# Kernel optimization log

Hardware: AMD Instinct MI355X
Metric: run time of the kernel (lower is better)

## Reference

```python
import jax, jax.numpy as jnp
import numpy as np

N_NODES = 50000
N_EDGES = 800000
N_FEAT = 128
HIDDEN = 128
N_CLASSES = 10
N_LAYERS = 3
N_GRAPHS = 512


def setup_inputs() -> dict:
    key = jax.random.key(0)
    ks = jax.random.split(key, 16)
    s = 1.0 / np.sqrt(HIDDEN)
    inp = {
        "x": jax.random.normal(ks[0], (N_NODES, N_FEAT), jnp.float32),
        "edge_index": jax.random.randint(ks[1], (2, N_EDGES), 0, N_NODES, jnp.int64),
        "batch": jnp.sort(jax.random.randint(ks[2], (N_NODES,), 0, N_GRAPHS, jnp.int64)),
        "num_graphs": N_GRAPHS,
        "conv1_wl": jax.random.normal(ks[3], (N_FEAT, HIDDEN), jnp.float32) * s,
        "conv1_wr": jax.random.normal(ks[4], (N_FEAT, HIDDEN), jnp.float32) * s,
        "conv1_b": jnp.zeros((HIDDEN,), jnp.float32),
        "convs_wl": jax.random.normal(ks[5], (N_LAYERS - 1, HIDDEN, HIDDEN), jnp.float32) * s,
        "convs_wr": jax.random.normal(ks[6], (N_LAYERS - 1, HIDDEN, HIDDEN), jnp.float32) * s,
        "convs_b": jnp.zeros((N_LAYERS - 1, HIDDEN), jnp.float32),
        "gate_w": jax.random.normal(ks[7], (HIDDEN, 1), jnp.float32) * s,
        "gate_b": jnp.zeros((1,), jnp.float32),
        "lin1_w": jax.random.normal(ks[8], (HIDDEN, HIDDEN), jnp.float32) * s,
        "lin1_b": jnp.zeros((HIDDEN,), jnp.float32),
        "lin2_w": jax.random.normal(ks[9], (HIDDEN, N_CLASSES), jnp.float32) * s,
        "lin2_b": jnp.zeros((N_CLASSES,), jnp.float32),
    }
    return inp


def _sage_conv(x, src, dst, inv_deg, wl, wr, b):
    # mean aggregation of source-node features at destination nodes
    agg = jax.ops.segment_sum(x[src], dst, num_segments=N_NODES)  # [N, d]
    agg = agg * inv_deg
    return agg @ wl + x @ wr + b


def _global_attention(x, batch, num_graphs, gate_w, gate_b):
    gate = (x @ gate_w + gate_b)[:, 0]                      # [N]
    m = jax.ops.segment_max(gate, batch, num_segments=num_graphs)
    m = jnp.where(jnp.isfinite(m), m, 0.0)
    g = jnp.exp(gate - m[batch])                            # stable segment softmax
    den = jax.ops.segment_sum(g, batch, num_segments=num_graphs)
    attn = g / den[batch]
    return jax.ops.segment_sum(attn[:, None] * x, batch, num_segments=num_graphs)


def reference(x, edge_index, batch, num_graphs,
              conv1_wl, conv1_wr, conv1_b,
              convs_wl, convs_wr, convs_b,
              gate_w, gate_b, lin1_w, lin1_b, lin2_w, lin2_b):
    src, dst = edge_index[0], edge_index[1]
    deg = jax.ops.segment_sum(jnp.ones((src.shape[0],), x.dtype), dst,
                              num_segments=N_NODES)
    inv_deg = (1.0 / jnp.maximum(deg, 1.0))[:, None]

    h = jax.nn.relu(_sage_conv(x, src, dst, inv_deg, conv1_wl, conv1_wr, conv1_b))
    for i in range(convs_wl.shape[0]):
        h = jax.nn.relu(_sage_conv(h, src, dst, inv_deg,
                                   convs_wl[i], convs_wr[i], convs_b[i]))

    pooled = _global_attention(h, batch, num_graphs, gate_w, gate_b)  # [G, H]
    out = jax.nn.relu(pooled @ lin1_w + lin1_b)
    # dropout p=0.5 is identity at eval time
    logits = out @ lin2_w + lin2_b
    return jax.nn.log_softmax(logits, axis=-1)
```

## Files before the change

### kernel.cpp

```cpp
#include <hip/hip_runtime.h>
#include <math.h>

#define N_NODES 50000
#define N_PAD   50048
#define N_EDGES 800000
#define FEAT 128
#define K2 256
#define N_GRAPHS 512
#define N_CLASSES 10
#define BCAP 64
#define RANGE_SZ 12500

typedef __attribute__((ext_vector_type(8))) short short8;
typedef __attribute__((ext_vector_type(4))) float floatx4;

__device__ __forceinline__ float bflo(unsigned u) { return __uint_as_float(u << 16); }
__device__ __forceinline__ float bfhi(unsigned u) { return __uint_as_float(u & 0xffff0000u); }
__device__ __forceinline__ unsigned short f2bf(float f) {
    unsigned u = __float_as_uint(f);
    u = (u + 0x7fffu + ((u >> 16) & 1u)) >> 16;
    return (unsigned short)u;
}
__device__ __forceinline__ unsigned pack2(float a, float b) {
    return (unsigned)f2bf(a) | ((unsigned)f2bf(b) << 16);
}
__device__ __forceinline__ unsigned fkey(float f) {
    unsigned b = __float_as_uint(f);
    return (b & 0x80000000u) ? ~b : (b | 0x80000000u);
}
__device__ __forceinline__ float fdecode(unsigned k) {
    unsigned b = (k & 0x80000000u) ? (k ^ 0x80000000u) : ~k;
    return __uint_as_float(b);
}

__global__ __launch_bounds__(256) void fill_bucket(
    const int* __restrict__ src, const int* __restrict__ dst,
    int* __restrict__ cnt, unsigned short* __restrict__ bucket) {
    int range = blockIdx.x & 3;
    int chunk = blockIdx.x >> 2;
    int e = chunk * 256 + threadIdx.x;
    int lo = range * RANGE_SZ;
    int d = dst[e];
    if (d >= lo && d < lo + RANGE_SZ) {
        int p = atomicAdd(&cnt[d], 1);
        if (p < BCAP) bucket[(size_t)d * BCAP + p] = (unsigned short)src[e];
    }
}

__global__ __launch_bounds__(256) void setup_kernel(
    const float* __restrict__ x, unsigned short* __restrict__ A,
    const float* __restrict__ wl1, const float* __restrict__ wr1,
    const float* __restrict__ wl23, const float* __restrict__ wr23,
    unsigned short* __restrict__ wt,
    const int* __restrict__ batch, int* __restrict__ goffs) {
    int b = blockIdx.x;
    if (b < 6250) {
        int idx = b * 256 + threadIdx.x;
        if (idx < N_NODES * 32) {
            int n = idx >> 5, f4 = idx & 31;
            float4 v = ((const float4*)(x + (size_t)n * FEAT))[f4];
            uint2 o = make_uint2(pack2(v.x, v.y), pack2(v.z, v.w));
            *(uint2*)(A + (size_t)n * K2 + FEAT + f4 * 4) = o;
        }
    } else if (b < 6250 + 384) {
        int idx = (b - 6250) * 256 + threadIdx.x;
        int layer = idx >> 15;
        int r = idx & 32767;
        int n = r >> 8, k = r & 255;
        const float* wl = (layer == 0) ? wl1 : wl23 + (size_t)(layer - 1) * FEAT * FEAT;
        const float* wr = (layer == 0) ? wr1 : wr23 + (size_t)(layer - 1) * FEAT * FEAT;
        float v = (k < FEAT) ? wl[k * FEAT + n] : wr[(k - FEAT) * FEAT + n];
        wt[idx] = f2bf(v);
    } else {
        int g = (b - 6250 - 384) * 256 + threadIdx.x;
        if (g > N_GRAPHS) return;
        int lo = 0, hi = N_NODES;
        while (lo < hi) {
            int mid = (lo + hi) >> 1;
            if (batch[mid] < g) lo = mid + 1; else hi = mid;
        }
        goffs[g] = lo;
    }
}

__device__ __forceinline__ void acc8(float* acc, uint4 u) {
    acc[0] += bflo(u.x); acc[1] += bfhi(u.x);
    acc[2] += bflo(u.y); acc[3] += bfhi(u.y);
    acc[4] += bflo(u.z); acc[5] += bfhi(u.z);
    acc[6] += bflo(u.w); acc[7] += bfhi(u.w);
}

__global__ __launch_bounds__(256) void aggregate_bf16(
    const unsigned short* __restrict__ hin, const int* __restrict__ cnt,
    const unsigned short* __restrict__ bucket, unsigned short* __restrict__ aggout) {
    int n = blockIdx.x * 4 + (threadIdx.x >> 6);
    if (n >= N_NODES) return;
    int lane = threadIdx.x & 63;
    int g = lane >> 4;
    int l16 = lane & 15;
    int deg = cnt[n];
    int c = min(deg, BCAP);
    int nq = c >> 2;
    int rem = c & 3;
    const unsigned short* cp = bucket + (size_t)n * BCAP;

    float acc[8];
    #pragma unroll
    for (int i = 0; i < 8; ++i) acc[i] = 0.f;

    int i = 0;
    for (; i + 4 <= nq; i += 4) {
        int s0 = cp[i * 4 + g];
        int s1 = cp[i * 4 + 4 + g];
        int s2 = cp[i * 4 + 8 + g];
        int s3 = cp[i * 4 + 12 + g];
        uint4 u0 = *(const uint4*)(hin + (size_t)s0 * K2 + l16 * 8);
        uint4 u1 = *(const uint4*)(hin + (size_t)s1 * K2 + l16 * 8);
        uint4 u2 = *(const uint4*)(hin + (size_t)s2 * K2 + l16 * 8);
        uint4 u3 = *(const uint4*)(hin + (size_t)s3 * K2 + l16 * 8);
        acc8(acc, u0); acc8(acc, u1); acc8(acc, u2); acc8(acc, u3);
    }
    if (i + 2 <= nq) {
        int s0 = cp[i * 4 + g];
        int s1 = cp[i * 4 + 4 + g];
        uint4 u0 = *(const uint4*)(hin + (size_t)s0 * K2 + l16 * 8);
        uint4 u1 = *(const uint4*)(hin + (size_t)s1 * K2 + l16 * 8);
        acc8(acc, u0); acc8(acc, u1);
        i += 2;
    }
    if (i < nq) {
        int s0 = cp[i * 4 + g];
        uint4 u0 = *(const uint4*)(hin + (size_t)s0 * K2 + l16 * 8);
        acc8(acc, u0);
    }
    if (g < rem) {
        int s0 = cp[nq * 4 + g];
        uint4 u0 = *(const uint4*)(hin + (size_t)s0 * K2 + l16 * 8);
        acc8(acc, u0);
    }
    #pragma unroll
    for (int j = 0; j < 8; ++j) {
        acc[j] += __shfl_xor(acc[j], 16);
        acc[j] += __shfl_xor(acc[j], 32);
    }
    if (g == 0) {
        float inv = 1.0f / fmaxf((float)deg, 1.0f);
        uint4 o;
        o.x = pack2(acc[0] * inv, acc[1] * inv);
        o.y = pack2(acc[2] * inv, acc[3] * inv);
        o.z = pack2(acc[4] * inv, acc[5] * inv);
        o.w = pack2(acc[6] * inv, acc[7] * inv);
        *(uint4*)(aggout + (size_t)n * K2 + l16 * 8) = o;
    }
}

__global__ __launch_bounds__(256) void gemm_mfma(
    unsigned short* __restrict__ A, const unsigned short* __restrict__ Wt,
    const float* __restrict__ bias,
    const float* __restrict__ gate_w, float* __restrict__ gate,
    unsigned* __restrict__ gmax, const int* __restrict__ batch) {
    int wave = threadIdx.x >> 6, lane = threadIdx.x & 63;
    int q = lane >> 4, l16 = lane & 15;
    int row0 = blockIdx.x * 128 + wave * 32;
    const unsigned short* pa0 = A + (size_t)(row0 + l16) * K2 + q * 8;
    const unsigned short* pa1 = pa0 + 16 * K2;
    const unsigned short* pb  = Wt + (size_t)l16 * K2 + q * 8;

    floatx4 acc[2][8];
    #pragma unroll
    for (int i = 0; i < 2; ++i)
        #pragma unroll
        for (int j = 0; j < 8; ++j) acc[i][j] = (floatx4){0.f, 0.f, 0.f, 0.f};

    #pragma unroll
    for (int ks = 0; ks < 8; ++ks) {
        short8 a0 = *(const short8*)(pa0 + ks * 32);
        short8 a1 = *(const short8*)(pa1 + ks * 32);
        #pragma unroll
        for (int nb = 0; nb < 8; ++nb) {
            short8 b = *(const short8*)(pb + (size_t)nb * 16 * K2 + ks * 32);
            acc[0][nb] = __builtin_amdgcn_mfma_f32_16x16x32_bf16(a0, b, acc[0][nb], 0, 0, 0);
            acc[1][nb] = __builtin_amdgcn_mfma_f32_16x16x32_bf16(a1, b, acc[1][nb], 0, 0, 0);
        }
    }

    float bv[8], gwv[8];
    #pragma unroll
    for (int nb = 0; nb < 8; ++nb) bv[nb] = bias[nb * 16 + l16];
    if (gate_w) {
        #pragma unroll
        for (int nb = 0; nb < 8; ++nb) gwv[nb] = gate_w[nb * 16 + l16];
    }

    #pragma unroll
    for (int band = 0; band < 2; ++band) {
        #pragma unroll
        for (int r = 0; r < 4; ++r) {
            int m = row0 + band * 16 + q * 4 + r;
            float gsum = 0.f;
            #pragma unroll
            for (int nb = 0; nb < 8; ++nb) {
                float v = fmaxf(acc[band][nb][r] + bv[nb], 0.f);
                if (m < N_NODES) A[(size_t)m * K2 + FEAT + nb * 16 + l16] = f2bf(v);
                if (gate_w) gsum += v * gwv[nb];
            }
            if (gate_w) {
                gsum += __shfl_xor(gsum, 1);
                gsum += __shfl_xor(gsum, 2);
                gsum += __shfl_xor(gsum, 4);
                gsum += __shfl_xor(gsum, 8);
                if (l16 == 0 && m < N_NODES) {
                    gate[m] = gsum;
                    atomicMax(&gmax[batch[m]], fkey(gsum));
                }
            }
        }
    }
}

__global__ __launch_bounds__(256) void pool_head(
    const unsigned short* __restrict__ h, const float* __restrict__ gate,
    const unsigned* __restrict__ gmax, const int* __restrict__ goffs,
    const float* __restrict__ w1, const float* __restrict__ b1,
    const float* __restrict__ w2, const float* __restrict__ b2,
    float* __restrict__ out) {
    __shared__ float sred[4];
    __shared__ float facc[4][128];
    __shared__ float pv[128], qv[128], lg[N_CLASSES];
    int g = blockIdx.x;
    int s = goffs[g], e = goffs[g + 1];
    int t = threadIdx.x;
    int wave = t >> 6, lane = t & 63;

    if (s < e) {
        float m = fdecode(gmax[g]);
        float d = 0.f;
        for (int n = s + t; n < e; n += 256) d += __expf(gate[n] - m);
        #pragma unroll
        for (int off = 32; off; off >>= 1) d += __shfl_xor(d, off);
        if (lane == 0) sred[wave] = d;
        __syncthreads();
        float den = sred[0] + sred[1] + sred[2] + sred[3];
        float acc0 = 0.f, acc1 = 0.f;
        for (int n = s + wave; n < e; n += 4) {
            float gn = __expf(gate[n] - m);
            unsigned u = *(const unsigned*)(h + (size_t)n * K2 + lane * 2);
            acc0 += gn * bflo(u);
            acc1 += gn * bfhi(u);
        }
        facc[wave][lane * 2]     = acc0;
        facc[wave][lane * 2 + 1] = acc1;
        __syncthreads();
        if (t < 128) pv[t] = (facc[0][t] + facc[1][t] + facc[2][t] + facc[3][t]) / den;
    } else {
        if (t < 128) pv[t] = 0.f;
    }
    __syncthreads();

    if (t < 128) {
        float acc = b1[t];
        #pragma unroll 4
        for (int k = 0; k < 128; ++k) acc += pv[k] * w1[k * FEAT + t];
        qv[t] = fmaxf(acc, 0.f);
    }
    __syncthreads();
    if (t < N_CLASSES) {
        float a = b2[t];
        #pragma unroll 4
        for (int k = 0; k < 128; ++k) a += qv[k] * w2[k * N_CLASSES + t];
        lg[t] = a;
    }
    __syncthreads();
    if (t < N_CLASSES) {
        float m = -INFINITY;
        #pragma unroll
        for (int j = 0; j < N_CLASSES; ++j) m = fmaxf(m, lg[j]);
        float sum = 0.f;
        #pragma unroll
        for (int j = 0; j < N_CLASSES; ++j) sum += __expf(lg[j] - m);
        out[(size_t)g * N_CLASSES + t] = lg[t] - m - __logf(sum);
    }
}

static inline size_t align256(size_t x) { return (x + 255) & ~(size_t)255; }

extern "C" void kernel_launch(void* const* d_in, const int* in_sizes, int n_in,
                              void* d_out, int out_size, void* d_ws, size_t ws_size,
                              hipStream_t stream) {
    const float* x        = (const float*)d_in[0];
    const int*   ei       = (const int*)d_in[1];
    const int*   batch    = (const int*)d_in[2];
    const float* conv1_wl = (const float*)d_in[4];
    const float* conv1_wr = (const float*)d_in[5];
    const float* conv1_b  = (const float*)d_in[6];
    const float* convs_wl = (const float*)d_in[7];
    const float* convs_wr = (const float*)d_in[8];
    const float* convs_b  = (const float*)d_in[9];
    const float* gate_w   = (const float*)d_in[10];
    const float* lin1_w   = (const float*)d_in[12];
    const float* lin1_b   = (const float*)d_in[13];
    const float* lin2_w   = (const float*)d_in[14];
    const float* lin2_b   = (const float*)d_in[15];
    float* out = (float*)d_out;

    const int* src = ei;
    const int* dst = ei + N_EDGES;

    char* w = (char*)d_ws;
    size_t off = 0;
    unsigned short* A1   = (unsigned short*)(w + off); off += align256((size_t)N_PAD * K2 * 2);
    unsigned short* bkt  = (unsigned short*)(w + off); off += align256((size_t)N_NODES * BCAP * 2);
    unsigned short* wt   = (unsigned short*)(w + off); off += align256((size_t)3 * FEAT * K2 * 2);
    float* f_gate = (float*)(w + off); off += align256((size_t)N_NODES * 4);
    int*   i_goff = (int*)(w + off);   off += align256((size_t)(N_GRAPHS + 1) * 4);
    char* zbase = w + off;
    int*      i_cnt  = (int*)(w + off);      off += align256((size_t)N_NODES * 4);
    unsigned* u_gmax = (unsigned*)(w + off); off += align256((size_t)N_GRAPHS * 4);
    size_t zbytes = (size_t)((w + off) - zbase);

    hipMemsetAsync(zbase, 0, zbytes, stream);

    fill_bucket<<<12500, 256, 0, stream>>>(src, dst, i_cnt, bkt);
    setup_kernel<<<6250 + 384 + 3, 256, 0, stream>>>(
        x, A1, conv1_wl, conv1_wr, convs_wl, convs_wr, wt, batch, i_goff);

    const int AB = (N_NODES + 3) / 4;
    const int GB = N_PAD / 128;

    aggregate_bf16<<<AB, 256, 0, stream>>>(A1 + FEAT, i_cnt, bkt, A1);
    gemm_mfma<<<GB, 256, 0, stream>>>(A1, wt, conv1_b,
                                      nullptr, nullptr, nullptr, nullptr);
    aggregate_bf16<<<AB, 256, 0, stream>>>(A1 + FEAT, i_cnt, bkt, A1);
    gemm_mfma<<<GB, 256, 0, stream>>>(A1, wt + FEAT * K2, convs_b,
                                      nullptr, nullptr, nullptr, nullptr);
    aggregate_bf16<<<AB, 256, 0, stream>>>(A1 + FEAT, i_cnt, bkt, A1);
    gemm_mfma<<<GB, 256, 0, stream>>>(A1, wt + 2 * FEAT * K2, convs_b + FEAT,
                                      gate_w, f_gate, u_gmax, batch);

    pool_head<<<N_GRAPHS, 256, 0, stream>>>(A1 + FEAT, f_gate, u_gmax, i_goff,
                                            lin1_w, lin1_b, lin2_w, lin2_b, out);
}
```

Before: 352.3 us.

## Make GEMM persistent with weights staged in LDS and prefetched A tiles

The GEMM kernel becomes persistent: 256 blocks loop over 64-row tiles. Each block copies the 128x256 bf16 weight matrix into padded shared memory once, instead of reading B fragments from global memory for every tile. The A fragments for the next tile are prefetched into registers while the current tile's MFMAs run. This cuts repeated weight traffic and launch granularity. In exchange it uses about 66KB of LDS per block, which limits occupancy, and it processes fewer rows per wave.

```diff
diff --git a/kernel.cpp b/kernel.cpp
--- a/kernel.cpp
+++ b/kernel.cpp
@@ -10,6 +10,10 @@
 #define N_CLASSES 10
 #define BCAP 64
 #define RANGE_SZ 12500
+#define WROW 264
+#define TILE_ROWS 64
+#define GEMM_BLOCKS 256
+#define N_TILES 782
 
 typedef __attribute__((ext_vector_type(8))) short short8;
 typedef __attribute__((ext_vector_type(4))) float floatx4;
@@ -159,29 +163,17 @@
     const float* __restrict__ bias,
     const float* __restrict__ gate_w, float* __restrict__ gate,
     unsigned* __restrict__ gmax, const int* __restrict__ batch) {
-    int wave = threadIdx.x >> 6, lane = threadIdx.x & 63;
+    __shared__ unsigned short sB[128 * WROW];
+    int t = threadIdx.x;
+    int wave = t >> 6, lane = t & 63;
     int q = lane >> 4, l16 = lane & 15;
-    int row0 = blockIdx.x * 128 + wave * 32;
-    const unsigned short* pa0 = A + (size_t)(row0 + l16) * K2 + q * 8;
-    const unsigned short* pa1 = pa0 + 16 * K2;
-    const unsigned short* pb  = Wt + (size_t)l16 * K2 + q * 8;
-
-    floatx4 acc[2][8];
+
     #pragma unroll
-    for (int i = 0; i < 2; ++i)
-        #pragma unroll
-        for (int j = 0; j < 8; ++j) acc[i][j] = (floatx4){0.f, 0.f, 0.f, 0.f};
-
-    #pragma unroll
-    for (int ks = 0; ks < 8; ++ks) {
-        short8 a0 = *(const short8*)(pa0 + ks * 32);
-        short8 a1 = *(const short8*)(pa1 + ks * 32);
-        #pragma unroll
-        for (int nb = 0; nb < 8; ++nb) {
-            short8 b = *(const short8*)(pb + (size_t)nb * 16 * K2 + ks * 32);
-            acc[0][nb] = __builtin_amdgcn_mfma_f32_16x16x32_bf16(a0, b, acc[0][nb], 0, 0, 0);
-            acc[1][nb] = __builtin_amdgcn_mfma_f32_16x16x32_bf16(a1, b, acc[1][nb], 0, 0, 0);
-        }
+    for (int i = 0; i < 16; ++i) {
+        int flat = i * 256 + t;
+        int rw = flat >> 5, fr = flat & 31;
+        uint4 v = *(const uint4*)(Wt + (size_t)flat * 8);
+        *(uint4*)(&sB[rw * WROW + fr * 8]) = v;
     }
 
     float bv[8], gwv[8];
@@ -192,15 +184,47 @@
         for (int nb = 0; nb < 8; ++nb) gwv[nb] = gate_w[nb * 16 + l16];
     }
 
-    #pragma unroll
-    for (int band = 0; band < 2; ++band) {
+    int tile = blockIdx.x;
+    short8 a[8];
+    {
+        const unsigned short* pa =
+            A + (size_t)(tile * TILE_ROWS + wave * 16 + l16) * K2 + q * 8;
+        #pragma unroll
+        for (int ks = 0; ks < 8; ++ks) a[ks] = *(const short8*)(pa + ks * 32);
+    }
+    __syncthreads();
+
+    while (tile < N_TILES) {
+        int ntile = tile + GEMM_BLOCKS;
+        short8 an[8];
+        if (ntile < N_TILES) {
+            const unsigned short* pa =
+                A + (size_t)(ntile * TILE_ROWS + wave * 16 + l16) * K2 + q * 8;
+            #pragma unroll
+            for (int ks = 0; ks < 8; ++ks) an[ks] = *(const short8*)(pa + ks * 32);
+        }
+
+        floatx4 acc[8];
+        #pragma unroll
+        for (int j = 0; j < 8; ++j) acc[j] = (floatx4){0.f, 0.f, 0.f, 0.f};
+
+        #pragma unroll
+        for (int ks = 0; ks < 8; ++ks) {
+            #pragma unroll
+            for (int nb = 0; nb < 8; ++nb) {
+                short8 b = *(const short8*)(&sB[(nb * 16 + l16) * WROW + ks * 32 + q * 8]);
+                acc[nb] = __builtin_amdgcn_mfma_f32_16x16x32_bf16(a[ks], b, acc[nb], 0, 0, 0);
+            }
+        }
+
+        int row0 = tile * TILE_ROWS + wave * 16;
         #pragma unroll
         for (int r = 0; r < 4; ++r) {
-            int m = row0 + band * 16 + q * 4 + r;
+            int m = row0 + q * 4 + r;
             float gsum = 0.f;
             #pragma unroll
             for (int nb = 0; nb < 8; ++nb) {
-                float v = fmaxf(acc[band][nb][r] + bv[nb], 0.f);
+                float v = fmaxf(acc[nb][r] + bv[nb], 0.f);
                 if (m < N_NODES) A[(size_t)m * K2 + FEAT + nb * 16 + l16] = f2bf(v);
                 if (gate_w) gsum += v * gwv[nb];
             }
@@ -215,6 +239,9 @@
                 }
             }
         }
+        tile = ntile;
+        #pragma unroll
+        for (int ks = 0; ks < 8; ++ks) a[ks] = an[ks];
     }
 }
 
@@ -325,17 +352,16 @@
         x, A1, conv1_wl, conv1_wr, convs_wl, convs_wr, wt, batch, i_goff);
 
     const int AB = (N_NODES + 3) / 4;
-    const int GB = N_PAD / 128;
 
     aggregate_bf16<<<AB, 256, 0, stream>>>(A1 + FEAT, i_cnt, bkt, A1);
-    gemm_mfma<<<GB, 256, 0, stream>>>(A1, wt, conv1_b,
-                                      nullptr, nullptr, nullptr, nullptr);
+    gemm_mfma<<<GEMM_BLOCKS, 256, 0, stream>>>(A1, wt, conv1_b,
+                                               nullptr, nullptr, nullptr, nullptr);
     aggregate_bf16<<<AB, 256, 0, stream>>>(A1 + FEAT, i_cnt, bkt, A1);
-    gemm_mfma<<<GB, 256, 0, stream>>>(A1, wt + FEAT * K2, convs_b,
-                                      nullptr, nullptr, nullptr, nullptr);
+    gemm_mfma<<<GEMM_BLOCKS, 256, 0, stream>>>(A1, wt + FEAT * K2, convs_b,
+                                               nullptr, nullptr, nullptr, nullptr);
     aggregate_bf16<<<AB, 256, 0, stream>>>(A1 + FEAT, i_cnt, bkt, A1);
-    gemm_mfma<<<GB, 256, 0, stream>>>(A1, wt + 2 * FEAT * K2, convs_b + FEAT,
-                                      gate_w, f_gate, u_gmax, batch);
+    gemm_mfma<<<GEMM_BLOCKS, 256, 0, stream>>>(A1, wt + 2 * FEAT * K2, convs_b + FEAT,
+                                               gate_w, f_gate, u_gmax, batch);
 
     pool_head<<<N_GRAPHS, 256, 0, stream>>>(A1 + FEAT, f_gate, u_gmax, i_goff,
                                             lin1_w, lin1_b, lin2_w, lin2_b, out);
```

Result: faster. 341.1 us (-3.2%).

## Split GEMM over N halves with LDS-staged weights, ping-pong buffers, coalesced stores

Applied to the files above, without the earlier changes.

The GEMM kernel now splits each 128-row tile into two blocks, one per 64-column half. It stages that half of the weights into LDS and preloads all A fragments into registers. Outputs go through an LDS tile so they can be written back as coalesced 16-byte rows, and ping-pong A buffers avoid the in-place read/write hazard. The per-graph gate max moves from atomicMax in the GEMM epilogue into pool_head, and gate partials are combined with atomicAdd across the two halves. This doubles the grid and adds LDS traffic and an extra workspace buffer in exchange for fewer scattered 2-byte global stores and no cross-block max atomics.

```diff
diff --git a/kernel.cpp b/kernel.cpp
--- a/kernel.cpp
+++ b/kernel.cpp
@@ -10,6 +10,8 @@
 #define N_CLASSES 10
 #define BCAP 64
 #define RANGE_SZ 12500
+#define BROW 264
+#define OROW 72
 
 typedef __attribute__((ext_vector_type(8))) short short8;
 typedef __attribute__((ext_vector_type(4))) float floatx4;
@@ -23,14 +25,6 @@
 }
 __device__ __forceinline__ unsigned pack2(float a, float b) {
     return (unsigned)f2bf(a) | ((unsigned)f2bf(b) << 16);
-}
-__device__ __forceinline__ unsigned fkey(float f) {
-    unsigned b = __float_as_uint(f);
-    return (b & 0x80000000u) ? ~b : (b | 0x80000000u);
-}
-__device__ __forceinline__ float fdecode(unsigned k) {
-    unsigned b = (k & 0x80000000u) ? (k ^ 0x80000000u) : ~k;
-    return __uint_as_float(b);
 }
 
 __global__ __launch_bounds__(256) void fill_bucket(
@@ -155,53 +149,70 @@
 }
 
 __global__ __launch_bounds__(256) void gemm_mfma(
-    unsigned short* __restrict__ A, const unsigned short* __restrict__ Wt,
-    const float* __restrict__ bias,
-    const float* __restrict__ gate_w, float* __restrict__ gate,
-    unsigned* __restrict__ gmax, const int* __restrict__ batch) {
-    int wave = threadIdx.x >> 6, lane = threadIdx.x & 63;
+    const unsigned short* __restrict__ Ain, unsigned short* __restrict__ Aout,
+    const unsigned short* __restrict__ Wt, const float* __restrict__ bias,
+    const float* __restrict__ gate_w, float* __restrict__ gate) {
+    __shared__ unsigned short sB[64 * BROW];
+    __shared__ unsigned short sOut[4][32 * OROW];
+    int t = threadIdx.x;
+    int wave = t >> 6, lane = t & 63;
     int q = lane >> 4, l16 = lane & 15;
-    int row0 = blockIdx.x * 128 + wave * 32;
-    const unsigned short* pa0 = A + (size_t)(row0 + l16) * K2 + q * 8;
+    int tileM = blockIdx.x >> 1;
+    int nh = blockIdx.x & 1;
+    int row0 = tileM * 128 + wave * 32;
+
+    const unsigned short* pa0 = Ain + (size_t)(row0 + l16) * K2 + q * 8;
     const unsigned short* pa1 = pa0 + 16 * K2;
-    const unsigned short* pb  = Wt + (size_t)l16 * K2 + q * 8;
-
-    floatx4 acc[2][8];
+    short8 a0[8], a1[8];
+    #pragma unroll
+    for (int ks = 0; ks < 8; ++ks) {
+        a0[ks] = *(const short8*)(pa0 + ks * 32);
+        a1[ks] = *(const short8*)(pa1 + ks * 32);
+    }
+
+    #pragma unroll
+    for (int i = 0; i < 8; ++i) {
+        int flat = i * 256 + t;
+        int rw = flat >> 5, fr = flat & 31;
+        uint4 v = *((const uint4*)(Wt + (size_t)(nh * 64 + rw) * K2) + fr);
+        *(uint4*)(&sB[rw * BROW + fr * 8]) = v;
+    }
+    __syncthreads();
+
+    floatx4 acc[2][4];
     #pragma unroll
     for (int i = 0; i < 2; ++i)
         #pragma unroll
-        for (int j = 0; j < 8; ++j) acc[i][j] = (floatx4){0.f, 0.f, 0.f, 0.f};
+        for (int j = 0; j < 4; ++j) acc[i][j] = (floatx4){0.f, 0.f, 0.f, 0.f};
 
     #pragma unroll
     for (int ks = 0; ks < 8; ++ks) {
-        short8 a0 = *(const short8*)(pa0 + ks * 32);
-        short8 a1 = *(const short8*)(pa1 + ks * 32);
-        #pragma unroll
-        for (int nb = 0; nb < 8; ++nb) {
-            short8 b = *(const short8*)(pb + (size_t)nb * 16 * K2 + ks * 32);
-            acc[0][nb] = __builtin_amdgcn_mfma_f32_16x16x32_bf16(a0, b, acc[0][nb], 0, 0, 0);
-            acc[1][nb] = __builtin_amdgcn_mfma_f32_16x16x32_bf16(a1, b, acc[1][nb], 0, 0, 0);
-        }
-    }
-
-    float bv[8], gwv[8];
-    #pragma unroll
-    for (int nb = 0; nb < 8; ++nb) bv[nb] = bias[nb * 16 + l16];
+        #pragma unroll
+        for (int nb = 0; nb < 4; ++nb) {
+            short8 b = *(const short8*)(&sB[(nb * 16 + l16) * BROW + ks * 32 + q * 8]);
+            acc[0][nb] = __builtin_amdgcn_mfma_f32_16x16x32_bf16(a0[ks], b, acc[0][nb], 0, 0, 0);
+            acc[1][nb] = __builtin_amdgcn_mfma_f32_16x16x32_bf16(a1[ks], b, acc[1][nb], 0, 0, 0);
+        }
+    }
+
+    float bv[4], gwv[4];
+    #pragma unroll
+    for (int nb = 0; nb < 4; ++nb) bv[nb] = bias[nh * 64 + nb * 16 + l16];
     if (gate_w) {
         #pragma unroll
-        for (int nb = 0; nb < 8; ++nb) gwv[nb] = gate_w[nb * 16 + l16];
+        for (int nb = 0; nb < 4; ++nb) gwv[nb] = gate_w[nh * 64 + nb * 16 + l16];
     }
 
     #pragma unroll
     for (int band = 0; band < 2; ++band) {
         #pragma unroll
         for (int r = 0; r < 4; ++r) {
-            int m = row0 + band * 16 + q * 4 + r;
+            int lr = band * 16 + q * 4 + r;
             float gsum = 0.f;
             #pragma unroll
-            for (int nb = 0; nb < 8; ++nb) {
+            for (int nb = 0; nb < 4; ++nb) {
                 float v = fmaxf(acc[band][nb][r] + bv[nb], 0.f);
-                if (m < N_NODES) A[(size_t)m * K2 + FEAT + nb * 16 + l16] = f2bf(v);
+                sOut[wave][lr * OROW + nb * 16 + l16] = f2bf(v);
                 if (gate_w) gsum += v * gwv[nb];
             }
             if (gate_w) {
@@ -209,18 +220,26 @@
                 gsum += __shfl_xor(gsum, 2);
                 gsum += __shfl_xor(gsum, 4);
                 gsum += __shfl_xor(gsum, 8);
-                if (l16 == 0 && m < N_NODES) {
-                    gate[m] = gsum;
-                    atomicMax(&gmax[batch[m]], fkey(gsum));
-                }
+                int m = row0 + lr;
+                if (l16 == 0 && m < N_NODES) atomicAdd(&gate[m], gsum);
             }
         }
+    }
+
+    int r2 = lane >> 1, h2 = lane & 1;
+    size_t gbase = (size_t)(row0 + r2) * K2 + FEAT + nh * 64 + h2 * 32;
+    #pragma unroll
+    for (int j = 0; j < 2; ++j) {
+        uint4 v0 = *(uint4*)(&sOut[wave][r2 * OROW + h2 * 32 + j * 16]);
+        uint4 v1 = *(uint4*)(&sOut[wave][r2 * OROW + h2 * 32 + j * 16 + 8]);
+        *(uint4*)(Aout + gbase + j * 16) = v0;
+        *(uint4*)(Aout + gbase + j * 16 + 8) = v1;
     }
 }
 
 __global__ __launch_bounds__(256) void pool_head(
     const unsigned short* __restrict__ h, const float* __restrict__ gate,
-    const unsigned* __restrict__ gmax, const int* __restrict__ goffs,
+    const int* __restrict__ goffs,
     const float* __restrict__ w1, const float* __restrict__ b1,
     const float* __restrict__ w2, const float* __restrict__ b2,
     float* __restrict__ out) {
@@ -233,7 +252,14 @@
     int wave = t >> 6, lane = t & 63;
 
     if (s < e) {
-        float m = fdecode(gmax[g]);
+        float mx = -INFINITY;
+        for (int n = s + t; n < e; n += 256) mx = fmaxf(mx, gate[n]);
+        #pragma unroll
+        for (int off = 32; off; off >>= 1) mx = fmaxf(mx, __shfl_xor(mx, off));
+        if (lane == 0) sred[wave] = mx;
+        __syncthreads();
+        float m = fmaxf(fmaxf(sred[0], sred[1]), fmaxf(sred[2], sred[3]));
+        __syncthreads();
         float d = 0.f;
         for (int n = s + t; n < e; n += 256) d += __expf(gate[n] - m);
         #pragma unroll
@@ -308,35 +334,33 @@
 
     char* w = (char*)d_ws;
     size_t off = 0;
+    unsigned short* A0   = (unsigned short*)(w + off); off += align256((size_t)N_PAD * K2 * 2);
     unsigned short* A1   = (unsigned short*)(w + off); off += align256((size_t)N_PAD * K2 * 2);
     unsigned short* bkt  = (unsigned short*)(w + off); off += align256((size_t)N_NODES * BCAP * 2);
     unsigned short* wt   = (unsigned short*)(w + off); off += align256((size_t)3 * FEAT * K2 * 2);
-    float* f_gate = (float*)(w + off); off += align256((size_t)N_NODES * 4);
     int*   i_goff = (int*)(w + off);   off += align256((size_t)(N_GRAPHS + 1) * 4);
     char* zbase = w + off;
-    int*      i_cnt  = (int*)(w + off);      off += align256((size_t)N_NODES * 4);
-    unsigned* u_gmax = (unsigned*)(w + off); off += align256((size_t)N_GRAPHS * 4);
+    int*   i_cnt  = (int*)(w + off);   off += align256((size_t)N_NODES * 4);
+    float* f_gate = (float*)(w + off); off += align256((size_t)N_NODES * 4);
     size_t zbytes = (size_t)((w + off) - zbase);
 
     hipMemsetAsync(zbase, 0, zbytes, stream);
 
     fill_bucket<<<12500, 256, 0, stream>>>(src, dst, i_cnt, bkt);
     setup_kernel<<<6250 + 384 + 3, 256, 0, stream>>>(
-        x, A1, conv1_wl, conv1_wr, convs_wl, convs_wr, wt, batch, i_goff);
+        x, A0, conv1_wl, conv1_wr, convs_wl, convs_wr, wt, batch, i_goff);
 
     const int AB = (N_NODES + 3) / 4;
-    const int GB = N_PAD / 128;
-
+    const int GB = (N_PAD / 128) * 2;
+
+    aggregate_bf16<<<AB, 256, 0, stream>>>(A0 + FEAT, i_cnt, bkt, A0);
+    gemm_mfma<<<GB, 256, 0, stream>>>(A0, A1, wt, conv1_b, nullptr, nullptr);
     aggregate_bf16<<<AB, 256, 0, stream>>>(A1 + FEAT, i_cnt, bkt, A1);
-    gemm_mfma<<<GB, 256, 0, stream>>>(A1, wt, conv1_b,
-                                      nullptr, nullptr, nullptr, nullptr);
-    aggregate_bf16<<<AB, 256, 0, stream>>>(A1 + FEAT, i_cnt, bkt, A1);
-    gemm_mfma<<<GB, 256, 0, stream>>>(A1, wt + FEAT * K2, convs_b,
-                                      nullptr, nullptr, nullptr, nullptr);
-    aggregate_bf16<<<AB, 256, 0, stream>>>(A1 + FEAT, i_cnt, bkt, A1);
-    gemm_mfma<<<GB, 256, 0, stream>>>(A1, wt + 2 * FEAT * K2, convs_b + FEAT,
-                                      gate_w, f_gate, u_gmax, batch);
-
-    pool_head<<<N_GRAPHS, 256, 0, stream>>>(A1 + FEAT, f_gate, u_gmax, i_goff,
+    gemm_mfma<<<GB, 256, 0, stream>>>(A1, A0, wt + FEAT * K2, convs_b, nullptr, nullptr);
+    aggregate_bf16<<<AB, 256, 0, stream>>>(A0 + FEAT, i_cnt, bkt, A0);
+    gemm_mfma<<<GB, 256, 0, stream>>>(A0, A1, wt + 2 * FEAT * K2, convs_b + FEAT,
+                                      gate_w, f_gate);
+
+    pool_head<<<N_GRAPHS, 256, 0, stream>>>(A1 + FEAT, f_gate, i_goff,
                                             lin1_w, lin1_b, lin2_w, lin2_b, out);
 }
```

Result: faster. 301.0 us, median of 2 (-14.6%).
